# Performance work log

Measured on AMD Instinct MI355X. Metric: run time of the kernel, lower is better.

The kernel has to match this reference:

```python
import jax, jax.numpy as jnp
import numpy as np

B, S, D, H = 2, 2048, 1024, 16
HD = D // H


def setup_inputs() -> dict:
    key = jax.random.key(0)
    ks = jax.random.split(key, 9)
    s = 1.0 / np.sqrt(D)
    inp = {
        "x": jax.random.normal(ks[0], (B, S, D), dtype=jnp.float32),
        "Wq": jax.random.uniform(ks[1], (D, D), jnp.float32, -s, s),
        "bq": jax.random.uniform(ks[2], (D,), jnp.float32, -s, s),
        "Wk": jax.random.uniform(ks[3], (D, D), jnp.float32, -s, s),
        "bk": jax.random.uniform(ks[4], (D,), jnp.float32, -s, s),
        "Wv": jax.random.uniform(ks[5], (D, D), jnp.float32, -s, s),
        "bv": jax.random.uniform(ks[6], (D,), jnp.float32, -s, s),
        "Wo": jax.random.uniform(ks[7], (D, D), jnp.float32, -s, s),
        "bo": jax.random.uniform(ks[8], (D,), jnp.float32, -s, s),
    }
    return inp


def reference(x, Wq, bq, Wk, bk, Wv, bv, Wo, bo):
    # Linear projections (torch Linear: y = x @ W.T + b)
    q = x @ Wq.T + bq  # [B,S,D]
    k = x @ Wk.T + bk
    v = x @ Wv.T + bv
    # split heads -> [B,H,S,HD]
    q = q.reshape(B, S, H, HD).transpose(0, 2, 1, 3)
    k = k.reshape(B, S, H, HD).transpose(0, 2, 1, 3)
    v = v.reshape(B, S, H, HD).transpose(0, 2, 1, 3)
    scores = jnp.einsum('bhqd,bhkd->bhqk', q, k) / jnp.sqrt(jnp.float32(HD))
    attn = jax.nn.softmax(scores, axis=-1)
    o = jnp.einsum('bhqk,bhkd->bhqd', attn, v)  # [B,H,S,HD]
    o = o.transpose(0, 2, 1, 3).reshape(B, S, D)
    return o @ Wo.T + bo
```

## Files before the change

kernel.cpp:

```cpp
#include <hip/hip_runtime.h>
#include <hip/hip_bf16.h>
#include <stdint.h>


typedef __attribute__((ext_vector_type(8))) short bf16x8;
typedef __attribute__((ext_vector_type(4))) float f32x4;
typedef __attribute__((ext_vector_type(4))) float floatx4;
typedef __attribute__((ext_vector_type(4))) short shortx4;

#define MFMA16(a, b, c) __builtin_amdgcn_mfma_f32_16x16x32_bf16((a), (b), (c), 0, 0, 0)

static __device__ __forceinline__ short f2bf(float f) {
  __hip_bfloat16 h = __float2bfloat16(f);
  return *reinterpret_cast<short*>(&h);
}

static __device__ __forceinline__ uint32_t pack_bf16(float a, float b) {
  return (uint32_t)(uint16_t)f2bf(a) | ((uint32_t)(uint16_t)f2bf(b) << 16);
}

static __device__ __forceinline__ float fexp2(float x) {
#if __has_builtin(__builtin_amdgcn_exp2f)
  return __builtin_amdgcn_exp2f(x);
#else
  return exp2f(x);
#endif
}

static __device__ __forceinline__ void gload_lds16(const void* g, void* l) {
  __builtin_amdgcn_global_load_lds(
      (__attribute__((address_space(1))) void*)(void*)g,
      (__attribute__((address_space(3))) void*)l, 16, 0, 0);
}

__global__ void convert_kernel(const float* __restrict__ x,
                               const float* __restrict__ Wq, const float* __restrict__ Wk,
                               const float* __restrict__ Wv, const float* __restrict__ Wo,
                               const float* __restrict__ bq, const float* __restrict__ bk,
                               const float* __restrict__ bv,
                               __hip_bfloat16* __restrict__ xb,
                               __hip_bfloat16* __restrict__ wqkv,
                               __hip_bfloat16* __restrict__ wob,
                               float* __restrict__ bcat) {
  const int NX = (4096 * 1024) / 4;
  const int NW = (1024 * 1024) / 4;
  const int total = NX + 4 * NW;
  for (long i = (long)blockIdx.x * blockDim.x + threadIdx.x; i < total + 768;
       i += (long)gridDim.x * blockDim.x) {
    if (i < total) {
      const float* src;
      __hip_bfloat16* dst;
      long off;
      if (i < NX)             { src = x;  dst = xb;                       off = i; }
      else if (i < NX + NW)   { src = Wq; dst = wqkv;                     off = i - NX; }
      else if (i < NX + 2*NW) { src = Wk; dst = wqkv + 1024 * 1024;       off = i - NX - NW; }
      else if (i < NX + 3*NW) { src = Wv; dst = wqkv + 2 * 1024 * 1024;   off = i - NX - 2*NW; }
      else                    { src = Wo; dst = wob;                      off = i - NX - 3*NW; }
      floatx4 v = *(const floatx4*)(src + off * 4);
      shortx4 sv;
      sv.x = f2bf(v.x); sv.y = f2bf(v.y); sv.z = f2bf(v.z); sv.w = f2bf(v.w);
      *(shortx4*)(dst + off * 4) = sv;
    } else {
      int j = (int)(i - total);
#pragma unroll
      for (int u = 0; u < 4; ++u) {
        int n = j * 4 + u;
        float b = (n < 1024) ? bq[n] : (n < 2048 ? bk[n - 1024] : bv[n - 2048]);
        bcat[n] = b;
      }
    }
  }
}

template <bool OUT_BF16>
__global__ __launch_bounds__(256, 2) void gemm_bt(const __hip_bfloat16* __restrict__ A,
                                                  const __hip_bfloat16* __restrict__ Bm,
                                                  const float* __restrict__ bias,
                                                  void* __restrict__ Cout, int M, int N, int K,
                                                  float scale, int scale_limit) {
  __shared__ __hip_bfloat16 As[128 * 64];
  __shared__ __hip_bfloat16 Bs[128 * 64];
  const int tid = threadIdx.x;
  const int lane = tid & 63;
  const int w = tid >> 6;
  const int wm = w >> 1, wn = w & 1;

  const int nwg = gridDim.x;
  const int bi = blockIdx.x;
  const int wg = (bi & 7) * (nwg >> 3) + (bi >> 3);
  const int MT = M >> 7;
  const int tm = wg % MT, tn = wg / MT;
  const long brow = (long)tm * 128, bcol = (long)tn * 128;

  const int srow = tid >> 3;
  const int scsw = (tid & 7) << 4;

  f32x4 acc[4][4] = {};

  char* lAs = (char*)As + (tid & 0xC0) * 16;
  char* lBs = (char*)Bs + (tid & 0xC0) * 16;

  for (int k0 = 0; k0 < K; k0 += 64) {
#pragma unroll
    for (int p = 0; p < 4; ++p) {
      int r = p * 32 + srow;
      int cb = scsw ^ ((r & 7) << 4);
      gload_lds16(A + (brow + r) * (long)K + k0 + (cb >> 1), lAs + p * 4096);
      gload_lds16(Bm + (bcol + r) * (long)K + k0 + (cb >> 1), lBs + p * 4096);
    }
    __syncthreads();
#pragma unroll
    for (int ks = 0; ks < 2; ++ks) {
      bf16x8 af[4], bfr[4];
      const int cbase = ks * 64 + ((lane >> 4) << 4);
#pragma unroll
      for (int m = 0; m < 4; ++m) {
        int r = wm * 64 + m * 16 + (lane & 15);
        af[m] = *(const bf16x8*)((const char*)As + r * 128 + (cbase ^ ((r & 7) << 4)));
      }
#pragma unroll
      for (int n = 0; n < 4; ++n) {
        int r = wn * 64 + n * 16 + (lane & 15);
        bfr[n] = *(const bf16x8*)((const char*)Bs + r * 128 + (cbase ^ ((r & 7) << 4)));
      }
#pragma unroll
      for (int m = 0; m < 4; ++m)
#pragma unroll
        for (int n = 0; n < 4; ++n) acc[m][n] = MFMA16(af[m], bfr[n], acc[m][n]);
    }
    __syncthreads();
  }

#pragma unroll
  for (int n = 0; n < 4; ++n) {
    const long col = bcol + wn * 64 + n * 16 + (lane & 15);
    const float bv = bias[col];
    const float sc = (col < scale_limit) ? scale : 1.0f;
#pragma unroll
    for (int m = 0; m < 4; ++m) {
      const long row0 = brow + wm * 64 + m * 16 + ((lane >> 4) << 2);
#pragma unroll
      for (int j = 0; j < 4; ++j) {
        float v = (acc[m][n][j] + bv) * sc;
        if (OUT_BF16)
          ((__hip_bfloat16*)Cout)[(row0 + j) * N + col] = __float2bfloat16(v);
        else
          ((float*)Cout)[(row0 + j) * N + col] = v;
      }
    }
  }
}

__global__ __launch_bounds__(256, 2) void attn_kernel(const __hip_bfloat16* __restrict__ qkv,
                                                      __hip_bfloat16* __restrict__ O) {
  __shared__ __hip_bfloat16 Ks[128 * 64];
  __shared__ __hip_bfloat16 Vt[64 * 128];

  const int tid = threadIdx.x;
  const int lane = tid & 63;
  const int w = tid >> 6;
  const int g = lane >> 4;
  const int t = lane & 15;
  const int bi = blockIdx.x;
  const int qt = bi & 15, hh = (bi >> 4) & 15, bb = bi >> 8;
  const long rowQ0 = (long)bb * 2048 + qt * 128;
  const long rowK0 = (long)bb * 2048;
  const int qcol = hh * 64, kcol = 1024 + hh * 64, vcol = 2048 + hh * 64;

  bf16x8 qf[2][2];
#pragma unroll
  for (int m = 0; m < 2; ++m)
#pragma unroll
    for (int ks = 0; ks < 2; ++ks) {
      long r = rowQ0 + w * 32 + m * 16 + t;
      int c = qcol + ks * 32 + g * 8;
      qf[m][ks] = *(const bf16x8*)(qkv + r * 3072 + c);
    }

  f32x4 acc_o[2][4] = {};
  float mrun[2] = {-1e30f, -1e30f}, lrun[2] = {0.f, 0.f};
  uint32_t cpk[2][8][2];

  const int sb = (lane & 48) | ((lane & 48) >> 2);

  const int srow = tid >> 3;
  const int scsw = (tid & 7) << 4;
  char* lKs = (char*)Ks + (tid & 0xC0) * 16;
  const int vr = tid >> 1;
  const int vc0 = (tid & 1) * 32;
  const int vphib = 4 * (vr >> 5) + ((vr >> 2) & 3);
  const int vinb = ((vr >> 4) & 1) * 8 + (vr & 3) * 2;

  for (int tt = 0; tt < 16; ++tt) {
    const long kv0 = (long)tt * 128;
#pragma unroll
    for (int p = 0; p < 4; ++p) {
      int r = p * 32 + srow;
      int cb = scsw ^ ((r & 7) << 4);
      gload_lds16(qkv + (rowK0 + kv0 + r) * 3072 + kcol + (cb >> 1), lKs + p * 4096);
    }
#pragma unroll
    for (int u = 0; u < 4; ++u) {
      bf16x8 v = *(const bf16x8*)(qkv + (rowK0 + kv0 + vr) * 3072 + vcol + vc0 + u * 8);
#pragma unroll
      for (int e = 0; e < 8; ++e) {
        int d = vc0 + u * 8 + e;
        *(short*)((char*)Vt + d * 256 + ((vphib ^ (d & 15)) << 4) + vinb) = v[e];
      }
    }
    __syncthreads();

#pragma unroll
    for (int m = 0; m < 2; ++m) {
      f32x4 s[8] = {};
#pragma unroll
      for (int ks = 0; ks < 2; ++ks) {
        const int cbase = ks * 64 + g * 16;
#pragma unroll
        for (int n = 0; n < 8; ++n) {
          int r = n * 16 + t;
          bf16x8 kf = *(const bf16x8*)((const char*)Ks + r * 128 + (cbase ^ ((r & 7) << 4)));
          s[n] = MFMA16(kf, qf[m][ks], s[n]);
        }
      }
      float mx = s[0][0];
#pragma unroll
      for (int n = 0; n < 8; ++n)
#pragma unroll
        for (int j = 0; j < 4; ++j) mx = fmaxf(mx, s[n][j]);
      mx = fmaxf(mx, __shfl_xor(mx, 16));
      mx = fmaxf(mx, __shfl_xor(mx, 32));
      const float newm = fmaxf(mrun[m], mx);
      const float corr = fexp2(mrun[m] - newm);
      mrun[m] = newm;
      float rs = 0.f;
#pragma unroll
      for (int n = 0; n < 8; ++n)
#pragma unroll
        for (int j = 0; j < 4; ++j) {
          float p = fexp2(s[n][j] - newm);
          s[n][j] = p;
          rs += p;
        }
      rs += __shfl_xor(rs, 16);
      rs += __shfl_xor(rs, 32);
      lrun[m] = lrun[m] * corr + rs;
#pragma unroll
      for (int j = 0; j < 4; ++j) {
        float cj = __shfl(corr, sb | j);
#pragma unroll
        for (int nd = 0; nd < 4; ++nd) acc_o[m][nd][j] *= cj;
      }
#pragma unroll
      for (int n = 0; n < 8; ++n) {
        cpk[m][n][0] = pack_bf16(s[n][0], s[n][1]);
        cpk[m][n][1] = pack_bf16(s[n][2], s[n][3]);
      }
    }

#pragma unroll
    for (int ks = 0; ks < 4; ++ks) {
      bf16x8 vf[4];
#pragma unroll
      for (int nd = 0; nd < 4; ++nd) {
        int d = nd * 16 + t;
        vf[nd] = *(const bf16x8*)((const char*)Vt + d * 256 + (((4 * ks + g) ^ t) << 4));
      }
#pragma unroll
      for (int m = 0; m < 2; ++m) {
        union { bf16x8 v; uint32_t u[4]; } au;
        au.u[0] = cpk[m][2 * ks][0];
        au.u[1] = cpk[m][2 * ks][1];
        au.u[2] = cpk[m][2 * ks + 1][0];
        au.u[3] = cpk[m][2 * ks + 1][1];
#pragma unroll
        for (int nd = 0; nd < 4; ++nd) acc_o[m][nd] = MFMA16(au.v, vf[nd], acc_o[m][nd]);
      }
    }
    __syncthreads();
  }

#pragma unroll
  for (int m = 0; m < 2; ++m) {
    const float inv = 1.0f / lrun[m];
#pragma unroll
    for (int j = 0; j < 4; ++j) {
      const float ij = __shfl(inv, sb | j);
      const long r = rowQ0 + w * 32 + m * 16 + g * 4 + j;
#pragma unroll
      for (int nd = 0; nd < 4; ++nd) {
        O[r * 1024 + qcol + nd * 16 + t] = __float2bfloat16(acc_o[m][nd][j] * ij);
      }
    }
  }
}

extern "C" void kernel_launch(void* const* d_in, const int* in_sizes, int n_in,
                              void* d_out, int out_size, void* d_ws, size_t ws_size,
                              hipStream_t stream) {
  const float* x  = (const float*)d_in[0];
  const float* Wq = (const float*)d_in[1];
  const float* bq = (const float*)d_in[2];
  const float* Wk = (const float*)d_in[3];
  const float* bk = (const float*)d_in[4];
  const float* Wv = (const float*)d_in[5];
  const float* bv = (const float*)d_in[6];
  const float* Wo = (const float*)d_in[7];
  const float* bo = (const float*)d_in[8];

  __hip_bfloat16* ws = (__hip_bfloat16*)d_ws;
  __hip_bfloat16* xb   = ws;
  __hip_bfloat16* wqkv = xb + (size_t)4096 * 1024;
  __hip_bfloat16* wob  = wqkv + (size_t)3072 * 1024;
  __hip_bfloat16* qkvb = wob + (size_t)1024 * 1024;
  __hip_bfloat16* ob   = qkvb + (size_t)4096 * 3072;
  float* bcat = (float*)(ob + (size_t)4096 * 1024);

  const float qscale = 0.18033688011112042f;

  convert_kernel<<<dim3(2048), dim3(256), 0, stream>>>(x, Wq, Wk, Wv, Wo, bq, bk, bv,
                                                       xb, wqkv, wob, bcat);
  gemm_bt<true><<<dim3(768), dim3(256), 0, stream>>>(xb, wqkv, bcat, (void*)qkvb,
                                                     4096, 3072, 1024, qscale, 1024);
  attn_kernel<<<dim3(512), dim3(256), 0, stream>>>(qkvb, ob);
  gemm_bt<false><<<dim3(256), dim3(256), 0, stream>>>(ob, wob, bo, d_out,
                                                      4096, 1024, 1024, 1.0f, 0);
}
```

Before: 198.6 us.

## Double-buffer K/V tiles in attention kernel to overlap loads with compute

Attention kernel now keeps two LDS buffers for K and transposed V. The next tile's K goes straight to LDS via async loads and its V is held in registers while the current tile is processed, which leaves one barrier per iteration instead of two. The QK^T loop is also restructured so each K fragment read feeds both m-rows. In exchange LDS use doubles to 64KB per block, which may limit the target two blocks per CU, and register pressure rises from vreg and s[2][8].

```diff
diff --git a/kernel.cpp b/kernel.cpp
--- a/kernel.cpp
+++ b/kernel.cpp
@@ -153,8 +153,8 @@
 
 __global__ __launch_bounds__(256, 2) void attn_kernel(const __hip_bfloat16* __restrict__ qkv,
                                                       __hip_bfloat16* __restrict__ O) {
-  __shared__ __hip_bfloat16 Ks[128 * 64];
-  __shared__ __hip_bfloat16 Vt[64 * 128];
+  __shared__ __hip_bfloat16 Ks[2][128 * 64];
+  __shared__ __hip_bfloat16 Vt[2][64 * 128];
 
   const int tid = threadIdx.x;
   const int lane = tid & 63;
@@ -185,49 +185,71 @@
 
   const int srow = tid >> 3;
   const int scsw = (tid & 7) << 4;
-  char* lKs = (char*)Ks + (tid & 0xC0) * 16;
   const int vr = tid >> 1;
   const int vc0 = (tid & 1) * 32;
   const int vphib = 4 * (vr >> 5) + ((vr >> 2) & 3);
   const int vinb = ((vr >> 4) & 1) * 8 + (vr & 3) * 2;
 
+  bf16x8 vreg[4];
+
+#pragma unroll
+  for (int p = 0; p < 4; ++p) {
+    int r = p * 32 + srow;
+    int cb = scsw ^ ((r & 7) << 4);
+    gload_lds16(qkv + (rowK0 + r) * 3072 + kcol + (cb >> 1),
+                (char*)(&Ks[0][0]) + (tid & 0xC0) * 16 + p * 4096);
+  }
+#pragma unroll
+  for (int u = 0; u < 4; ++u)
+    vreg[u] = *(const bf16x8*)(qkv + (rowK0 + vr) * 3072 + vcol + vc0 + u * 8);
+#pragma unroll
+  for (int u = 0; u < 4; ++u)
+#pragma unroll
+    for (int e = 0; e < 8; ++e) {
+      int d = vc0 + u * 8 + e;
+      *(short*)((char*)(&Vt[0][0]) + d * 256 + ((vphib ^ (d & 15)) << 4) + vinb) = vreg[u][e];
+    }
+  __syncthreads();
+
+  int cur = 0;
   for (int tt = 0; tt < 16; ++tt) {
-    const long kv0 = (long)tt * 128;
-#pragma unroll
-    for (int p = 0; p < 4; ++p) {
-      int r = p * 32 + srow;
-      int cb = scsw ^ ((r & 7) << 4);
-      gload_lds16(qkv + (rowK0 + kv0 + r) * 3072 + kcol + (cb >> 1), lKs + p * 4096);
-    }
-#pragma unroll
-    for (int u = 0; u < 4; ++u) {
-      bf16x8 v = *(const bf16x8*)(qkv + (rowK0 + kv0 + vr) * 3072 + vcol + vc0 + u * 8);
-#pragma unroll
-      for (int e = 0; e < 8; ++e) {
-        int d = vc0 + u * 8 + e;
-        *(short*)((char*)Vt + d * 256 + ((vphib ^ (d & 15)) << 4) + vinb) = v[e];
-      }
-    }
-    __syncthreads();
+    if (tt < 15) {
+      const long kvn = (long)(tt + 1) * 128;
+#pragma unroll
+      for (int p = 0; p < 4; ++p) {
+        int r = p * 32 + srow;
+        int cb = scsw ^ ((r & 7) << 4);
+        gload_lds16(qkv + (rowK0 + kvn + r) * 3072 + kcol + (cb >> 1),
+                    (char*)(&Ks[cur ^ 1][0]) + (tid & 0xC0) * 16 + p * 4096);
+      }
+#pragma unroll
+      for (int u = 0; u < 4; ++u)
+        vreg[u] = *(const bf16x8*)(qkv + (rowK0 + kvn + vr) * 3072 + vcol + vc0 + u * 8);
+    }
+
+    const char* KsCur = (const char*)(&Ks[cur][0]);
+    const char* VtCur = (const char*)(&Vt[cur][0]);
+
+    f32x4 s[2][8] = {};
+#pragma unroll
+    for (int ks = 0; ks < 2; ++ks) {
+      const int cbase = ks * 64 + g * 16;
+#pragma unroll
+      for (int n = 0; n < 8; ++n) {
+        const int r = n * 16 + t;
+        const bf16x8 kf = *(const bf16x8*)(KsCur + r * 128 + (cbase ^ ((r & 7) << 4)));
+        s[0][n] = MFMA16(kf, qf[0][ks], s[0][n]);
+        s[1][n] = MFMA16(kf, qf[1][ks], s[1][n]);
+      }
+    }
 
 #pragma unroll
     for (int m = 0; m < 2; ++m) {
-      f32x4 s[8] = {};
-#pragma unroll
-      for (int ks = 0; ks < 2; ++ks) {
-        const int cbase = ks * 64 + g * 16;
-#pragma unroll
-        for (int n = 0; n < 8; ++n) {
-          int r = n * 16 + t;
-          bf16x8 kf = *(const bf16x8*)((const char*)Ks + r * 128 + (cbase ^ ((r & 7) << 4)));
-          s[n] = MFMA16(kf, qf[m][ks], s[n]);
-        }
-      }
-      float mx = s[0][0];
+      float mx = s[m][0][0];
 #pragma unroll
       for (int n = 0; n < 8; ++n)
 #pragma unroll
-        for (int j = 0; j < 4; ++j) mx = fmaxf(mx, s[n][j]);
+        for (int j = 0; j < 4; ++j) mx = fmaxf(mx, s[m][n][j]);
       mx = fmaxf(mx, __shfl_xor(mx, 16));
       mx = fmaxf(mx, __shfl_xor(mx, 32));
       const float newm = fmaxf(mrun[m], mx);
@@ -238,8 +260,8 @@
       for (int n = 0; n < 8; ++n)
 #pragma unroll
         for (int j = 0; j < 4; ++j) {
-          float p = fexp2(s[n][j] - newm);
-          s[n][j] = p;
+          float p = fexp2(s[m][n][j] - newm);
+          s[m][n][j] = p;
           rs += p;
         }
       rs += __shfl_xor(rs, 16);
@@ -253,8 +275,8 @@
       }
 #pragma unroll
       for (int n = 0; n < 8; ++n) {
-        cpk[m][n][0] = pack_bf16(s[n][0], s[n][1]);
-        cpk[m][n][1] = pack_bf16(s[n][2], s[n][3]);
+        cpk[m][n][0] = pack_bf16(s[m][n][0], s[m][n][1]);
+        cpk[m][n][1] = pack_bf16(s[m][n][2], s[m][n][3]);
       }
     }
 
@@ -264,7 +286,7 @@
 #pragma unroll
       for (int nd = 0; nd < 4; ++nd) {
         int d = nd * 16 + t;
-        vf[nd] = *(const bf16x8*)((const char*)Vt + d * 256 + (((4 * ks + g) ^ t) << 4));
+        vf[nd] = *(const bf16x8*)(VtCur + d * 256 + (((4 * ks + g) ^ t) << 4));
       }
 #pragma unroll
       for (int m = 0; m < 2; ++m) {
@@ -277,7 +299,19 @@
         for (int nd = 0; nd < 4; ++nd) acc_o[m][nd] = MFMA16(au.v, vf[nd], acc_o[m][nd]);
       }
     }
-    __syncthreads();
+
+    if (tt < 15) {
+      char* VtNxt = (char*)(&Vt[cur ^ 1][0]);
+#pragma unroll
+      for (int u = 0; u < 4; ++u)
+#pragma unroll
+        for (int e = 0; e < 8; ++e) {
+          int d = vc0 + u * 8 + e;
+          *(short*)(VtNxt + d * 256 + ((vphib ^ (d & 15)) << 4) + vinb) = vreg[u][e];
+        }
+      __syncthreads();
+      cur ^= 1;
+    }
   }
 
 #pragma unroll
```

After: 200.3 us. No clear change (+0.9%).
